# Kernel tuning notes

Measured on AMD Instinct MI355X. Metric: run time of the kernel, lower is better.

Reference implementation:

```python
import jax, jax.numpy as jnp
import numpy as np
from functools import partial

V, E, H, F = 32000, 256, 512, 256  # vocab, embed_dim, hidden_dim, num_filters
FS = (3, 4, 5)

def setup_inputs() -> dict:
    key = jax.random.key(0)
    ks = jax.random.split(key, 24)
    s = 0.02
    d = {}
    d["src"] = jax.random.randint(ks[0], (32, 512), 0, V)
    d["trg"] = jax.random.randint(ks[1], (32, 64), 0, V)
    # embeddings with padding_idx=0 zeroed
    d["enc_emb"] = (jax.random.normal(ks[2], (V, E)) * s).at[0].set(0.0)
    d["dec_emb"] = (jax.random.normal(ks[3], (V, E)) * s).at[0].set(0.0)
    # conv1d weights (out_channels=F, in_channels=E, kernel)
    d["conv_w3"] = jax.random.normal(ks[4], (F, E, 3)) * s
    d["conv_b3"] = jnp.zeros((F,))
    d["conv_w4"] = jax.random.normal(ks[5], (F, E, 4)) * s
    d["conv_b4"] = jnp.zeros((F,))
    d["conv_w5"] = jax.random.normal(ks[6], (F, E, 5)) * s
    d["conv_b5"] = jnp.zeros((F,))
    d["fc1_w"] = jax.random.normal(ks[7], (H, 3 * F)) * s
    d["fc1_b"] = jnp.zeros((H,))
    d["fc2_w"] = jax.random.normal(ks[8], (H, H)) * s
    d["fc2_b"] = jnp.zeros((H,))
    # 2-layer LSTM: layer1 input E+H, layer2 input H; gates order i,f,g,o
    d["w_ih1"] = jax.random.normal(ks[9], (4 * H, E + H)) * s
    d["w_hh1"] = jax.random.normal(ks[10], (4 * H, H)) * s
    d["b_ih1"] = jnp.zeros((4 * H,))
    d["b_hh1"] = jnp.zeros((4 * H,))
    d["w_ih2"] = jax.random.normal(ks[11], (4 * H, H)) * s
    d["w_hh2"] = jax.random.normal(ks[12], (4 * H, H)) * s
    d["b_ih2"] = jnp.zeros((4 * H,))
    d["b_hh2"] = jnp.zeros((4 * H,))
    d["out_w"] = jax.random.normal(ks[13], (V, H)) * s
    d["out_b"] = jnp.zeros((V,))
    return d

def _lstm_cell(x, h, c, w_ih, w_hh, b_ih, b_hh):
    gates = x @ w_ih.T + b_ih + h @ w_hh.T + b_hh  # (B, 4H)
    i, f, g, o = jnp.split(gates, 4, axis=-1)
    c_new = jax.nn.sigmoid(f) * c + jax.nn.sigmoid(i) * jnp.tanh(g)
    h_new = jax.nn.sigmoid(o) * jnp.tanh(c_new)
    return h_new, c_new

def _encoder(src, enc_emb, convs, fc1_w, fc1_b, fc2_w, fc2_b):
    x = enc_emb[src]                    # (B, S, E)
    x = jnp.transpose(x, (0, 2, 1))     # (B, E, S)
    pooled = []
    for w, b in convs:
        y = jax.lax.conv_general_dilated(
            x, w, window_strides=(1,), padding='VALID',
            dimension_numbers=('NCH', 'OIH', 'NCH'))  # (B, F, S-k+1)
        pooled.append(jnp.max(jax.nn.relu(y + b[None, :, None]), axis=2))
    cat = jnp.concatenate(pooled, axis=1)              # (B, 3F)
    h = jax.nn.relu(cat @ fc1_w.T + fc1_b)             # (B, H)
    return h @ fc2_w.T + fc2_b                         # (B, H)

def reference(src, trg, enc_emb, conv_w3, conv_b3, conv_w4, conv_b4,
              conv_w5, conv_b5, fc1_w, fc1_b, fc2_w, fc2_b, dec_emb,
              w_ih1, w_hh1, b_ih1, b_hh1, w_ih2, w_hh2, b_ih2, b_hh2,
              out_w, out_b):
    B, T = trg.shape
    enc_out = _encoder(src, enc_emb,
                       [(conv_w3, conv_b3), (conv_w4, conv_b4), (conv_w5, conv_b5)],
                       fc1_w, fc1_b, fc2_w, fc2_b)  # (B, H)

    def step(carry, tok):
        h1, c1, h2, c2 = carry
        x = jnp.concatenate([dec_emb[tok], enc_out], axis=1)  # (B, E+H)
        h1, c1 = _lstm_cell(x, h1, c1, w_ih1, w_hh1, b_ih1, b_hh1)
        h2, c2 = _lstm_cell(h1, h2, c2, w_ih2, w_hh2, b_ih2, b_hh2)
        logits = h2 @ out_w.T + out_b                          # (B, V)
        return (h1, c1, h2, c2), logits

    z = jnp.zeros((B, H), dtype=enc_out.dtype)
    tokens = trg[:, :-1].T  # teacher forcing (ratio=1.0): (T-1, B)
    _, logits = jax.lax.scan(step, (z, z, z, z), tokens)       # (T-1, B, V)
    logits = jnp.transpose(logits, (1, 0, 2))                  # (B, T-1, V)
    # outputs[:, 0] is left as zeros, matching the torch loop starting at t=1
    return jnp.concatenate([jnp.zeros((B, 1, logits.shape[-1]), logits.dtype), logits], axis=1)
```

## Files before the change

kernel.cpp:

```cpp
#include <hip/hip_runtime.h>
#include <math.h>
#include <stdint.h>

#define B_    32
#define E_    256
#define F_    256
#define H_    512
#define V_    32000
#define G4    2048

typedef unsigned short u16;
typedef unsigned long long u64;
typedef __attribute__((ext_vector_type(8))) short bf16x8;
typedef __attribute__((ext_vector_type(4))) float f32x4;

__device__ __forceinline__ float fsig(float x) {
  return __builtin_amdgcn_rcpf(1.f + __expf(-x));
}
__device__ __forceinline__ float ftanh(float x) {
  return 1.f - 2.f * __builtin_amdgcn_rcpf(1.f + __expf(2.f * x));
}

__device__ __forceinline__ u16 f2bf(float f) {
  uint32_t u = __float_as_uint(f);
  uint32_t r = (u + 0x7FFFu + ((u >> 16) & 1u)) >> 16;
  return (u16)r;
}
__device__ __forceinline__ uint32_t pack2(float a, float b) {
  return (uint32_t)f2bf(a) | ((uint32_t)f2bf(b) << 16);
}

#define GLOAD16(gp, lp) __builtin_amdgcn_global_load_lds( \
    (const __attribute__((address_space(1))) uint32_t*)(const void*)(gp), \
    (__attribute__((address_space(3))) uint32_t*)(void*)(lp), 16, 0, 0)

#define ALOAD(P) __hip_atomic_load((P), __ATOMIC_RELAXED, __HIP_MEMORY_SCOPE_AGENT)
#define ASTORE(P, V) __hip_atomic_store((P), (V), __ATOMIC_RELAXED, __HIP_MEMORY_SCOPE_AGENT)

__global__ void init_all(float* pooled, uint32_t* sent1, uint32_t* sent2,
                         uint32_t* cnt1, u16* h1d, u16* h2a,
                         const float* bi1, const float* bh1,
                         const float* bi2, const float* bh2,
                         float* bs1, float* bs2, float* out) {
  int i = blockIdx.x * blockDim.x + threadIdx.x, st = gridDim.x * blockDim.x;
  for (int k = i; k < 24576; k += st) pooled[k] = 0.f;
  for (int k = i; k < 131072; k += st) {
    uint32_t v = (k < 2048 && (k & 15) == 0) ? 1u : 0u;
    sent1[k] = v; sent2[k] = v;
  }
  for (int k = i; k < 256; k += st) cnt1[k] = 0u;
  uint4 z = {0u, 0u, 0u, 0u};
  for (int k = i; k < 2048; k += st) { ((uint4*)h1d)[k] = z; ((uint4*)h2a)[k] = z; }
  for (int k = i; k < G4; k += st) { bs1[k] = bi1[k] + bh1[k]; bs2[k] = bi2[k] + bh2[k]; }
  for (int k = i; k < B_ * V_; k += st) {
    int b = k / V_, v = k - b * V_;
    __builtin_nontemporal_store(0.f, &out[(size_t)b * 64 * V_ + v]);
  }
}

__global__ void cvt_all(const float* s0, u16* d0, const float* s1, u16* d1,
                        const float* s2, u16* d2, const float* s3, u16* d3,
                        const float* s4, u16* d4) {
  int i = blockIdx.x * blockDim.x + threadIdx.x, st = gridDim.x * blockDim.x;
  for (; i < 2637824; i += st) {
    int j = i; const float* s; u16* d;
    if (j < 2048000) { s = s0; d = d0; }
    else if ((j -= 2048000) < 196608) { s = s1; d = d1; }
    else if ((j -= 196608) < 131072) { s = s2; d = d2; }
    else if ((j -= 131072) < 131072) { s = s3; d = d3; }
    else { j -= 131072; s = s4; d = d4; }
    const float4* sp = (const float4*)s + 2 * (size_t)j;
    float4 a = sp[0], b = sp[1];
    uint4 u;
    u.x = pack2(a.x, a.y); u.y = pack2(a.z, a.w);
    u.z = pack2(b.x, b.y); u.w = pack2(b.z, b.w);
    *((uint4*)d + j) = u;
  }
}

__global__ void wtj_all(const float* w3, u16* t3, const float* w4, u16* t4,
                        const float* w5, u16* t5) {
  int i = blockIdx.x * blockDim.x + threadIdx.x, st = gridDim.x * blockDim.x;
  for (; i < 786432; i += st) {
    int j = i; const float* w; u16* wt; int kw;
    if (j < 196608) { w = w3; wt = t3; kw = 3; }
    else if ((j -= 196608) < 262144) { w = w4; wt = t4; kw = 4; }
    else { j -= 262144; w = w5; wt = t5; kw = 5; }
    int f = j / (kw * 256);
    int r = j - f * (kw * 256);
    int jj = r >> 8, e = r & 255;
    wt[j] = f2bf(w[(f * 256 + e) * kw + jj]);
  }
}

__global__ void gemm_small(const float* __restrict__ A, const float* __restrict__ W,
                           const float* __restrict__ bias, float* __restrict__ C,
                           int K, int N, int relu) {
  int nl = threadIdx.x & 7, b = threadIdx.x >> 3;
  int n = blockIdx.x * 8 + nl;
  const float* a = A + b * K;
  const float* w = W + (size_t)n * K;
  float acc = 0.f;
  for (int k = 0; k < K; k += 4) {
    float4 av = *reinterpret_cast<const float4*>(&a[k]);
    float4 wv = *reinterpret_cast<const float4*>(&w[k]);
    acc = fmaf(av.x, wv.x, acc); acc = fmaf(av.y, wv.y, acc);
    acc = fmaf(av.z, wv.z, acc); acc = fmaf(av.w, wv.w, acc);
  }
  acc += bias[n];
  if (relu) acc = fmaxf(acc, 0.f);
  C[b * N + n] = acc;
}

__global__ __launch_bounds__(256)
void conv_mfma(const u16* __restrict__ wt3, const u16* __restrict__ wt4,
               const u16* __restrict__ wt5,
               const float* __restrict__ cb3, const float* __restrict__ cb4,
               const float* __restrict__ cb5,
               float* __restrict__ pooled,
               const int* __restrict__ srcTok, const float* __restrict__ emb) {
  const int z = blockIdx.z;
  const u16* Bw = (z == 0) ? wt3 : (z == 1) ? wt4 : wt5;
  const float* bias = (z == 0) ? cb3 : (z == 1) ? cb4 : cb5;
  const int K = 768 + 256 * z, kw = 3 + z, poolOff = 256 * z;

  __shared__ char smem[32768];
  const int tid = threadIdx.x;
  const int wid = tid >> 6, lane = tid & 63;
  const int hi = lane >> 4, lo = lane & 15;
  const int wr = wid >> 1, wc = wid & 1;
  const int m0 = blockIdx.x * 128, n0 = blockIdx.y * 128;
  const int NT = K >> 5;
  const int srow = lane >> 2, sc = lane & 3;

  f32x4 acc[4][4];
#pragma unroll
  for (int i = 0; i < 4; ++i)
#pragma unroll
    for (int j = 0; j < 4; ++j) acc[i][j] = (f32x4){0.f, 0.f, 0.f, 0.f};

  for (int t = -1; t < NT; ++t) {
    int ts = t + 1;
    if (ts < NT) {
      char* base = smem + (ts & 1) * 16384;
      int k0 = ts << 5;
      {
        int j = k0 >> 8, e0 = k0 & 255;
        int row = tid >> 1;
        int m = m0 + row;
        int s = m & 511, b = m >> 9;
        int sj = s + j;
        int tok = (sj < 512) ? srcTok[b * 512 + sj] : -1;
#pragma unroll
        for (int q = 0; q < 2; ++q) {
          int cg = (tid & 1) * 2 + q;
          uint4 u;
          if (tok >= 0) {
            const float* ep = emb + (size_t)tok * 256 + e0 + cg * 8;
            float4 f0 = *(const float4*)(ep);
            float4 f1 = *(const float4*)(ep + 4);
            u.x = pack2(f0.x, f0.y); u.y = pack2(f0.z, f0.w);
            u.z = pack2(f1.x, f1.y); u.w = pack2(f1.z, f1.w);
          } else u = (uint4){0, 0, 0, 0};
          int c = cg ^ (row & 3);
          *(uint4*)(base + row * 64 + c * 16) = u;
        }
      }
#pragma unroll
      for (int q = 0; q < 2; ++q) {
        int row = (wid + q * 4) * 16 + srow;
        int gc = sc ^ (row & 3);
        const char* gp = (const char*)Bw + (((size_t)(n0 + row) * K + k0) << 1) + gc * 16;
        GLOAD16(gp, base + 8192 + (wid + q * 4) * 1024);
      }
    }
    if (t >= 0) {
      char* base = smem + (t & 1) * 16384;
      bf16x8 af[4], bfr[4];
#pragma unroll
      for (int mi = 0; mi < 4; ++mi) {
        int row = wr * 64 + mi * 16 + lo;
        af[mi] = *(const bf16x8*)(base + row * 64 + ((hi ^ (row & 3)) << 4));
      }
#pragma unroll
      for (int ni = 0; ni < 4; ++ni) {
        int row = wc * 64 + ni * 16 + lo;
        bfr[ni] = *(const bf16x8*)(base + 8192 + row * 64 + ((hi ^ (row & 3)) << 4));
      }
#pragma unroll
      for (int mi = 0; mi < 4; ++mi)
#pragma unroll
        for (int ni = 0; ni < 4; ++ni)
          acc[mi][ni] = __builtin_amdgcn_mfma_f32_16x16x32_bf16(af[mi], bfr[ni], acc[mi][ni], 0, 0, 0);
    }
    __syncthreads();
  }

  int b = m0 >> 9;
  int slim = 512 - kw;
#pragma unroll
  for (int ni = 0; ni < 4; ++ni) {
    int col = n0 + wc * 64 + ni * 16 + lo;
    float bv = bias[col];
    float mx = 0.f;
#pragma unroll
    for (int mi = 0; mi < 4; ++mi)
#pragma unroll
      for (int r = 0; r < 4; ++r) {
        int m = m0 + wr * 64 + mi * 16 + hi * 4 + r;
        int s = m & 511;
        float v = acc[mi][ni][r] + bv;
        if (s <= slim && v > mx) mx = v;
      }
    atomicMax((int*)&pooled[b * 768 + poolOff + col], __float_as_int(mx));
  }
}

__global__ __launch_bounds__(256, 1)
void lstm_fused(float* __restrict__ pre,
                const u16* __restrict__ whh1,
                const u16* __restrict__ wih2, const u16* __restrict__ whh2,
                const float* __restrict__ bs2,
                uint32_t* __restrict__ sent1, uint32_t* __restrict__ sent2,
                uint32_t* __restrict__ cnt1,
                u16* __restrict__ h1d, u16* __restrict__ h2a,
                const u16* __restrict__ outw_bf, const float* __restrict__ outb,
                float* __restrict__ out,
                const int* __restrict__ trg, const float* __restrict__ demb,
                const float* __restrict__ enco,
                const u16* __restrict__ wih1_bf, const float* __restrict__ bs1) {
  __shared__ char smem[74752];
  const int tid = threadIdx.x;
  const int wid = tid >> 6, lane = tid & 63, hi = lane >> 4, lo = lane & 15;
  const int hrow = tid >> 3, k8 = tid & 7;
  const int pb = hrow, pj0 = k8 * 2;

#define WAVE_DRAIN() asm volatile("s_waitcnt vmcnt(0)" ::: "memory")
#define POLL1(P) while (ALOAD(P) == 0u) __builtin_amdgcn_s_sleep(1);
#define POLL2(P, Q) for (;;) { uint32_t x_ = ALOAD(P), y_ = ALOAD(Q); \
                               if (x_ & y_) break; __builtin_amdgcn_s_sleep(1); }
#define POLL2S(P, Q) for (;;) { uint32_t x_ = ALOAD(P), y_ = ALOAD(Q); \
                                if (x_ & y_) break; __builtin_amdgcn_s_sleep(16); }

  if (blockIdx.x < 32) {
    const int bi = blockIdx.x;
    u16* hlds = (u16*)smem;
    float* glds = (float*)(smem + 33280);

    bf16x8 wreg[16];
    const u16* wp = whh1 + (((size_t)(wid * 512 + bi * 16 + lo)) << 9) + hi * 8;
#pragma unroll
    for (int ks = 0; ks < 16; ++ks) wreg[ks] = *(const bf16x8*)(wp + ks * 32);

    float creg0 = 0.f, creg1 = 0.f;

    for (int t = 0; t < 63; ++t) {
      if ((t & 3) == 0) {
        if (tid == 0)
          while (ALOAD(cnt1 + (t >> 2) * 16) < 16u) __builtin_amdgcn_s_sleep(8);
        __syncthreads();
      }
      const float* pr = pre + (((size_t)(t * 32 + pb)) << 11) + bi * 16 + pj0;
      float pi0 = pr[0], pf0 = pr[512], pg0 = pr[1024], po0 = pr[1536];
      float pi1 = pr[1], pf1 = pr[513], pg1 = pr[1025], po1 = pr[1537];

      const u64* hp = (const u64*)(h1d + ((size_t)t * 32 + hrow) * 512);
      f32x4 acc0 = (f32x4){0.f,0.f,0.f,0.f}, acc1 = (f32x4){0.f,0.f,0.f,0.f};

      POLL1(sent1 + (size_t)t * 2048 + lane * 16)
      {
        u64 v[8];
#pragma unroll
        for (int g = 0; g < 4; ++g) {
          int c = k8 + 8 * g;
          v[2*g]   = ALOAD(hp + 2 * c);
          v[2*g+1] = ALOAD(hp + 2 * c + 1);
        }
#pragma unroll
        for (int g = 0; g < 4; ++g) {
          int c = k8 + 8 * g;
          u64 w2[2] = { v[2*g], v[2*g+1] };
          *(uint4*)(hlds + hrow * 520 + c * 8) = *(const uint4*)w2;
        }
      }
      __syncthreads();
#pragma unroll
      for (int ks = 0; ks < 8; ++ks) {
        int cg = (ks * 4 + hi) * 8;
        bf16x8 a0 = *(const bf16x8*)(hlds + lo * 520 + cg);
        bf16x8 a1 = *(const bf16x8*)(hlds + (16 + lo) * 520 + cg);
        acc0 = __builtin_amdgcn_mfma_f32_16x16x32_bf16(a0, wreg[ks], acc0, 0, 0, 0);
        acc1 = __builtin_amdgcn_mfma_f32_16x16x32_bf16(a1, wreg[ks], acc1, 0, 0, 0);
      }
      POLL1(sent1 + (size_t)t * 2048 + (64 + lane) * 16)
      {
        u64 v[8];
#pragma unroll
        for (int g = 0; g < 4; ++g) {
          int c = 32 + k8 + 8 * g;
          v[2*g]   = ALOAD(hp + 2 * c);
          v[2*g+1] = ALOAD(hp + 2 * c + 1);
        }
#pragma unroll
        for (int g = 0; g < 4; ++g) {
          int c = 32 + k8 + 8 * g;
          u64 w2[2] = { v[2*g], v[2*g+1] };
          *(uint4*)(hlds + hrow * 520 + c * 8) = *(const uint4*)w2;
        }
      }
      __syncthreads();
#pragma unroll
      for (int ks = 8; ks < 16; ++ks) {
        int cg = (ks * 4 + hi) * 8;
        bf16x8 a0 = *(const bf16x8*)(hlds + lo * 520 + cg);
        bf16x8 a1 = *(const bf16x8*)(hlds + (16 + lo) * 520 + cg);
        acc0 = __builtin_amdgcn_mfma_f32_16x16x32_bf16(a0, wreg[ks], acc0, 0, 0, 0);
        acc1 = __builtin_amdgcn_mfma_f32_16x16x32_bf16(a1, wreg[ks], acc1, 0, 0, 0);
      }
#pragma unroll
      for (int r = 0; r < 4; ++r) {
        glds[wid * 544 + (hi * 4 + r) * 17 + lo] = acc0[r];
        glds[wid * 544 + (16 + hi * 4 + r) * 17 + lo] = acc1[r];
      }
      __syncthreads();

      float iv0 = glds[0*544 + pb*17 + pj0]   + pi0, fv0 = glds[1*544 + pb*17 + pj0]   + pf0;
      float gv0 = glds[2*544 + pb*17 + pj0]   + pg0, ov0 = glds[3*544 + pb*17 + pj0]   + po0;
      float iv1 = glds[0*544 + pb*17 + pj0+1] + pi1, fv1 = glds[1*544 + pb*17 + pj0+1] + pf1;
      float gv1 = glds[2*544 + pb*17 + pj0+1] + pg1, ov1 = glds[3*544 + pb*17 + pj0+1] + po1;
      float cn0 = fsig(fv0) * creg0 + fsig(iv0) * ftanh(gv0);
      float hn0 = fsig(ov0) * ftanh(cn0);
      float cn1 = fsig(fv1) * creg1 + fsig(iv1) * ftanh(gv1);
      float hn1 = fsig(ov1) * ftanh(cn1);
      creg0 = cn0; creg1 = cn1;
      ASTORE((uint32_t*)(h1d + ((size_t)(t + 1) * 32 + pb) * 512 + bi * 16 + pj0),
             pack2(hn0, hn1));
      WAVE_DRAIN();
      if (lane == 0)
        ASTORE(sent1 + (size_t)(t + 1) * 2048 + (bi * 4 + wid) * 16, 1u);
    }
  } else if (blockIdx.x < 64) {
    const int bi2 = blockIdx.x - 32;
    u16* alds = (u16*)smem;
    float* glds = (float*)(smem + 66048);

    bf16x8 wreg[32];
    {
      const u16* wa = wih2 + (((size_t)(wid * 512 + bi2 * 16 + lo)) << 9) + hi * 8;
      const u16* wb = whh2 + (((size_t)(wid * 512 + bi2 * 16 + lo)) << 9) + hi * 8;
#pragma unroll
      for (int ks = 0; ks < 16; ++ks) {
        wreg[ks]      = *(const bf16x8*)(wa + ks * 32);
        wreg[16 + ks] = *(const bf16x8*)(wb + ks * 32);
      }
    }
    float bsv0 = bs2[0 * 512 + bi2 * 16 + pj0], bsv0b = bs2[0 * 512 + bi2 * 16 + pj0 + 1];
    float bsv1 = bs2[1 * 512 + bi2 * 16 + pj0], bsv1b = bs2[1 * 512 + bi2 * 16 + pj0 + 1];
    float bsv2 = bs2[2 * 512 + bi2 * 16 + pj0], bsv2b = bs2[2 * 512 + bi2 * 16 + pj0 + 1];
    float bsv3 = bs2[3 * 512 + bi2 * 16 + pj0], bsv3b = bs2[3 * 512 + bi2 * 16 + pj0 + 1];

    float creg0 = 0.f, creg1 = 0.f;

    for (int t = 0; t < 63; ++t) {
      f32x4 acc0 = (f32x4){0.f,0.f,0.f,0.f}, acc1 = (f32x4){0.f,0.f,0.f,0.f};

      POLL2(sent1 + (size_t)(t + 1) * 2048 + lane * 16,
            sent1 + (size_t)(t + 1) * 2048 + (64 + lane) * 16)
      {
        const u64* hp1 = (const u64*)(h1d + ((size_t)(t + 1) * 32 + hrow) * 512);
        u64 v[16];
#pragma unroll
        for (int g = 0; g < 8; ++g) {
          int c = k8 + 8 * g;
          v[2*g]   = ALOAD(hp1 + 2 * c);
          v[2*g+1] = ALOAD(hp1 + 2 * c + 1);
        }
#pragma unroll
        for (int g = 0; g < 8; ++g) {
          int c = k8 + 8 * g;
          u64 w2[2] = { v[2*g], v[2*g+1] };
          *(uint4*)(alds + hrow * 1032 + c * 8) = *(const uint4*)w2;
        }
      }
      __syncthreads();
#pragma unroll
      for (int ks = 0; ks < 16; ++ks) {
        int cg = (ks * 4 + hi) * 8;
        bf16x8 a0 = *(const bf16x8*)(alds + lo * 1032 + cg);
        bf16x8 a1 = *(const bf16x8*)(alds + (16 + lo) * 1032 + cg);
        acc0 = __builtin_amdgcn_mfma_f32_16x16x32_bf16(a0, wreg[ks], acc0, 0, 0, 0);
        acc1 = __builtin_amdgcn_mfma_f32_16x16x32_bf16(a1, wreg[ks], acc1, 0, 0, 0);
      }
      POLL2(sent2 + (size_t)t * 2048 + lane * 16,
            sent2 + (size_t)t * 2048 + (64 + lane) * 16)
      {
        const u64* hp2 = (const u64*)(h2a + ((size_t)t * 32 + hrow) * 512);
        u64 v[16];
#pragma unroll
        for (int g = 0; g < 8; ++g) {
          int c = k8 + 8 * g;
          v[2*g]   = ALOAD(hp2 + 2 * c);
          v[2*g+1] = ALOAD(hp2 + 2 * c + 1);
        }
#pragma unroll
        for (int g = 0; g < 8; ++g) {
          int c = 64 + k8 + 8 * g;
          u64 w2[2] = { v[2*g], v[2*g+1] };
          *(uint4*)(alds + hrow * 1032 + c * 8) = *(const uint4*)w2;
        }
      }
      __syncthreads();
#pragma unroll
      for (int ks = 0; ks < 16; ++ks) {
        int cg = (64 + ks * 4 + hi) * 8;
        bf16x8 a0 = *(const bf16x8*)(alds + lo * 1032 + cg);
        bf16x8 a1 = *(const bf16x8*)(alds + (16 + lo) * 1032 + cg);
        acc0 = __builtin_amdgcn_mfma_f32_16x16x32_bf16(a0, wreg[16 + ks], acc0, 0, 0, 0);
        acc1 = __builtin_amdgcn_mfma_f32_16x16x32_bf16(a1, wreg[16 + ks], acc1, 0, 0, 0);
      }
#pragma unroll
      for (int r = 0; r < 4; ++r) {
        glds[wid * 544 + (hi * 4 + r) * 17 + lo] = acc0[r];
        glds[wid * 544 + (16 + hi * 4 + r) * 17 + lo] = acc1[r];
      }
      __syncthreads();

      float gi0 = glds[0*544 + pb*17 + pj0]   + bsv0,  gf0 = glds[1*544 + pb*17 + pj0]   + bsv1;
      float gg0 = glds[2*544 + pb*17 + pj0]   + bsv2,  go0 = glds[3*544 + pb*17 + pj0]   + bsv3;
      float gi1 = glds[0*544 + pb*17 + pj0+1] + bsv0b, gf1 = glds[1*544 + pb*17 + pj0+1] + bsv1b;
      float gg1 = glds[2*544 + pb*17 + pj0+1] + bsv2b, go1 = glds[3*544 + pb*17 + pj0+1] + bsv3b;
      float cn0 = fsig(gf0) * creg0 + fsig(gi0) * ftanh(gg0);
      float hn0 = fsig(go0) * ftanh(cn0);
      float cn1 = fsig(gf1) * creg1 + fsig(gi1) * ftanh(gg1);
      float hn1 = fsig(go1) * ftanh(cn1);
      creg0 = cn0; creg1 = cn1;
      ASTORE((uint32_t*)(h2a + ((size_t)(t + 1) * 32 + pb) * 512 + bi2 * 16 + pj0),
             pack2(hn0, hn1));
      WAVE_DRAIN();
      if (lane == 0)
        ASTORE(sent2 + (size_t)(t + 1) * 2048 + (bi2 * 4 + wid) * 16, 1u);
    }
  } else {
    const int bid2 = blockIdx.x - 64;
    const int wr = wid >> 1, wc = wid & 1;
    const int srow = lane >> 2, sc = lane & 3;

    for (int w = bid2; w < 256; w += 160) {
      int rt = w >> 4, ct = w & 15;
      const int m0 = rt * 128, n0 = ct * 128;
      f32x4 acc[4][4];
#pragma unroll
      for (int i = 0; i < 4; ++i)
#pragma unroll
        for (int j = 0; j < 4; ++j) acc[i][j] = (f32x4){0.f, 0.f, 0.f, 0.f};

      for (int t = -1; t < 24; ++t) {
        int ts = t + 1;
        if (ts < 24) {
          char* base = smem + (ts & 1) * 16384;
          int k0 = ts << 5;
          {
            int row = tid >> 1;
            int m = m0 + row;
            int tt = m >> 5, b = m & 31;
            int ok = (m < 2016);
            int tok = ok ? trg[b * 64 + tt] : 0;
#pragma unroll
            for (int q = 0; q < 2; ++q) {
              int cg = (tid & 1) * 2 + q;
              int k = k0 + cg * 8;
              uint4 u;
              if (ok) {
                const float* ep = (k < 256) ? (demb + (size_t)tok * 256 + k)
                                            : (enco + (size_t)b * 512 + (k - 256));
                float4 f0 = *(const float4*)(ep);
                float4 f1 = *(const float4*)(ep + 4);
                u.x = pack2(f0.x, f0.y); u.y = pack2(f0.z, f0.w);
                u.z = pack2(f1.x, f1.y); u.w = pack2(f1.z, f1.w);
              } else u = (uint4){0, 0, 0, 0};
              int c = cg ^ (row & 3);
              *(uint4*)(base + row * 64 + c * 16) = u;
            }
          }
#pragma unroll
          for (int q = 0; q < 2; ++q) {
            int row = (wid + q * 4) * 16 + srow;
            int gc = sc ^ (row & 3);
            const char* gp = (const char*)wih1_bf + (((size_t)(n0 + row) * 768 + k0) << 1) + gc * 16;
            GLOAD16(gp, base + 8192 + (wid + q * 4) * 1024);
          }
        }
        if (t >= 0) {
          char* base = smem + (t & 1) * 16384;
          bf16x8 af[4], bfr[4];
#pragma unroll
          for (int mi = 0; mi < 4; ++mi) {
            int row = wr * 64 + mi * 16 + lo;
            af[mi] = *(const bf16x8*)(base + row * 64 + ((hi ^ (row & 3)) << 4));
          }
#pragma unroll
          for (int ni = 0; ni < 4; ++ni) {
            int row = wc * 64 + ni * 16 + lo;
            bfr[ni] = *(const bf16x8*)(base + 8192 + row * 64 + ((hi ^ (row & 3)) << 4));
          }
#pragma unroll
          for (int mi = 0; mi < 4; ++mi)
#pragma unroll
            for (int ni = 0; ni < 4; ++ni)
              acc[mi][ni] = __builtin_amdgcn_mfma_f32_16x16x32_bf16(af[mi], bfr[ni], acc[mi][ni], 0, 0, 0);
        }
        __syncthreads();
      }
#pragma unroll
      for (int mi = 0; mi < 4; ++mi)
#pragma unroll
        for (int r = 0; r < 4; ++r) {
          int m = m0 + wr * 64 + mi * 16 + hi * 4 + r;
          if (m >= 2016) continue;
#pragma unroll
          for (int ni = 0; ni < 4; ++ni) {
            int col = n0 + wc * 64 + ni * 16 + lo;
            ASTORE((uint32_t*)(pre + (size_t)m * 2048 + col),
                   __float_as_uint(acc[mi][ni][r] + bs1[col]));
          }
        }
      WAVE_DRAIN();
      __syncthreads();
      if (tid == 0)
        __hip_atomic_fetch_add(cnt1 + rt * 16, 1u, __ATOMIC_RELAXED, __HIP_MEMORY_SCOPE_AGENT);
      __syncthreads();
    }

    const u16* A = h2a + 16384;

    for (int w = bid2; w < 16 * 250; w += 160) {
      int rt = w / 250, ct = w - rt * 250;
      int tf = rt * 4 + 4; if (tf > 63) tf = 63;
      if (wid == 0)
        POLL2S(sent2 + (size_t)tf * 2048 + lane * 16,
               sent2 + (size_t)tf * 2048 + (64 + lane) * 16)
      __syncthreads();

      const int m0 = rt * 128, n0 = ct * 128;
      f32x4 acc[4][4];
#pragma unroll
      for (int i = 0; i < 4; ++i)
#pragma unroll
        for (int j = 0; j < 4; ++j) acc[i][j] = (f32x4){0.f, 0.f, 0.f, 0.f};

      for (int t = -1; t < 16; ++t) {
        int ts = t + 1;
        if (ts < 16) {
          char* base = smem + (ts & 1) * 16384;
          int k0 = ts << 5;
#pragma unroll
          for (int q = 0; q < 2; ++q) {
            int row = (wid + q * 4) * 16 + srow;
            int gc = sc ^ (row & 3);
            const char* gp = (const char*)A + (((size_t)(m0 + row) * 512 + k0) << 1) + gc * 16;
            GLOAD16(gp, base + (wid + q * 4) * 1024);
          }
#pragma unroll
          for (int q = 0; q < 2; ++q) {
            int row = (wid + q * 4) * 16 + srow;
            int gc = sc ^ (row & 3);
            const char* gp = (const char*)outw_bf + (((size_t)(n0 + row) * 512 + k0) << 1) + gc * 16;
            GLOAD16(gp, base + 8192 + (wid + q * 4) * 1024);
          }
        }
        if (t >= 0) {
          char* base = smem + (t & 1) * 16384;
          bf16x8 af[4], bfr[4];
#pragma unroll
          for (int mi = 0; mi < 4; ++mi) {
            int row = wr * 64 + mi * 16 + lo;
            af[mi] = *(const bf16x8*)(base + row * 64 + ((hi ^ (row & 3)) << 4));
          }
#pragma unroll
          for (int ni = 0; ni < 4; ++ni) {
            int row = wc * 64 + ni * 16 + lo;
            bfr[ni] = *(const bf16x8*)(base + 8192 + row * 64 + ((hi ^ (row & 3)) << 4));
          }
#pragma unroll
          for (int mi = 0; mi < 4; ++mi)
#pragma unroll
            for (int ni = 0; ni < 4; ++ni)
              acc[mi][ni] = __builtin_amdgcn_mfma_f32_16x16x32_bf16(af[mi], bfr[ni], acc[mi][ni], 0, 0, 0);
        }
        __syncthreads();
      }

#pragma unroll
      for (int mi = 0; mi < 4; ++mi)
#pragma unroll
        for (int r = 0; r < 4; ++r) {
          int m = m0 + wr * 64 + mi * 16 + hi * 4 + r;
          if (m >= 2016) continue;
          int t2 = m >> 5, b = m & 31;
          size_t rowbase = ((size_t)b * 64 + t2 + 1) * (size_t)V_;
#pragma unroll
          for (int ni = 0; ni < 4; ++ni) {
            int col = n0 + wc * 64 + ni * 16 + lo;
            __builtin_nontemporal_store(acc[mi][ni][r] + outb[col], &out[rowbase + col]);
          }
        }
    }
  }
#undef POLL1
#undef POLL2
#undef POLL2S
#undef WAVE_DRAIN
}

extern "C" void kernel_launch(void* const* d_in, const int* in_sizes, int n_in,
                              void* d_out, int out_size, void* d_ws, size_t ws_size,
                              hipStream_t stream) {
  const int*   src  = (const int*)  d_in[0];
  const int*   trg  = (const int*)  d_in[1];
  const float* eemb = (const float*)d_in[2];
  const float* demb = (const float*)d_in[3];
  const float* cw3  = (const float*)d_in[4];
  const float* cb3  = (const float*)d_in[5];
  const float* cw4  = (const float*)d_in[6];
  const float* cb4  = (const float*)d_in[7];
  const float* cw5  = (const float*)d_in[8];
  const float* cb5  = (const float*)d_in[9];
  const float* fc1w = (const float*)d_in[10];
  const float* fc1b = (const float*)d_in[11];
  const float* fc2w = (const float*)d_in[12];
  const float* fc2b = (const float*)d_in[13];
  const float* wih1 = (const float*)d_in[14];
  const float* whh1 = (const float*)d_in[15];
  const float* bih1 = (const float*)d_in[16];
  const float* bhh1 = (const float*)d_in[17];
  const float* wih2 = (const float*)d_in[18];
  const float* whh2 = (const float*)d_in[19];
  const float* bih2 = (const float*)d_in[20];
  const float* bhh2 = (const float*)d_in[21];
  const float* outw = (const float*)d_in[22];
  const float* outb = (const float*)d_in[23];
  float* out = (float*)d_out;

  uint32_t* sent1 = (uint32_t*)d_ws;
  uint32_t* sent2 = sent1 + 131072;
  uint32_t* cnt1  = sent2 + 131072;
  u16* h1d      = (u16*)(cnt1 + 256);
  u16* h2a      = h1d + 1048576;
  float* pooled = (float*)(h2a + 1048576);
  float* ench   = pooled + 24576;
  float* enco   = ench + 16384;
  float* bs1    = enco + 16384;
  float* bs2    = bs1 + 2048;
  float* pre    = bs2 + 2048;
  u16* outw_bf  = (u16*)(pre + 4128768);
  u16* wih1_bf  = outw_bf + 16384000;
  u16* wih2_bf  = wih1_bf + 1572864;
  u16* whh1_bf  = wih2_bf + 1048576;
  u16* whh2_bf  = whh1_bf + 1048576;
  u16* wtj3     = whh2_bf + 1048576;
  u16* wtj4     = wtj3 + 196608;
  u16* wtj5     = wtj4 + 262144;

  init_all<<<512, 256, 0, stream>>>(pooled, sent1, sent2, cnt1, h1d, h2a,
                                    bih1, bhh1, bih2, bhh2, bs1, bs2, out);
  cvt_all<<<2048, 256, 0, stream>>>(outw, outw_bf, wih1, wih1_bf, wih2, wih2_bf,
                                    whh1, whh1_bf, whh2, whh2_bf);
  wtj_all<<<512, 256, 0, stream>>>(cw3, wtj3, cw4, wtj4, cw5, wtj5);

  conv_mfma<<<dim3(128, 2, 3), 256, 0, stream>>>(wtj3, wtj4, wtj5, cb3, cb4, cb5,
                                                 pooled, src, eemb);
  gemm_small<<<64, 256, 0, stream>>>(pooled, fc1w, fc1b, ench, 768, 512, 1);
  gemm_small<<<64, 256, 0, stream>>>(ench, fc2w, fc2b, enco, 512, 512, 0);

  lstm_fused<<<224, 256, 0, stream>>>(pre, whh1_bf, wih2_bf, whh2_bf, bs2,
                                      sent1, sent2, cnt1, h1d, h2a,
                                      outw_bf, outb, out,
                                      trg, demb, enco, wih1_bf, bs1);
}
```

Baseline: 467.3 us.

## Merge prep kernels and make output-GEMM blocks own column tiles

Result: slower. 576.7 us (+23.4%).

```diff
diff --git a/kernel.cpp b/kernel.cpp
--- a/kernel.cpp
+++ b/kernel.cpp
@@ -37,33 +37,19 @@
 #define ALOAD(P) __hip_atomic_load((P), __ATOMIC_RELAXED, __HIP_MEMORY_SCOPE_AGENT)
 #define ASTORE(P, V) __hip_atomic_store((P), (V), __ATOMIC_RELAXED, __HIP_MEMORY_SCOPE_AGENT)
 
-__global__ void init_all(float* pooled, uint32_t* sent1, uint32_t* sent2,
+__global__ void prep_all(float* pooled, uint32_t* sent1, uint32_t* sent2,
                          uint32_t* cnt1, u16* h1d, u16* h2a,
                          const float* bi1, const float* bh1,
                          const float* bi2, const float* bh2,
-                         float* bs1, float* bs2, float* out) {
+                         float* bs1, float* bs2, float* out,
+                         const float* s0, u16* d0, const float* s1, u16* d1,
+                         const float* s2, u16* d2, const float* s3, u16* d3,
+                         const float* s4, u16* d4,
+                         const float* w3, u16* t3, const float* w4, u16* t4,
+                         const float* w5, u16* t5) {
   int i = blockIdx.x * blockDim.x + threadIdx.x, st = gridDim.x * blockDim.x;
-  for (int k = i; k < 24576; k += st) pooled[k] = 0.f;
-  for (int k = i; k < 131072; k += st) {
-    uint32_t v = (k < 2048 && (k & 15) == 0) ? 1u : 0u;
-    sent1[k] = v; sent2[k] = v;
-  }
-  for (int k = i; k < 256; k += st) cnt1[k] = 0u;
-  uint4 z = {0u, 0u, 0u, 0u};
-  for (int k = i; k < 2048; k += st) { ((uint4*)h1d)[k] = z; ((uint4*)h2a)[k] = z; }
-  for (int k = i; k < G4; k += st) { bs1[k] = bi1[k] + bh1[k]; bs2[k] = bi2[k] + bh2[k]; }
-  for (int k = i; k < B_ * V_; k += st) {
-    int b = k / V_, v = k - b * V_;
-    __builtin_nontemporal_store(0.f, &out[(size_t)b * 64 * V_ + v]);
-  }
-}
-
-__global__ void cvt_all(const float* s0, u16* d0, const float* s1, u16* d1,
-                        const float* s2, u16* d2, const float* s3, u16* d3,
-                        const float* s4, u16* d4) {
-  int i = blockIdx.x * blockDim.x + threadIdx.x, st = gridDim.x * blockDim.x;
-  for (; i < 2637824; i += st) {
-    int j = i; const float* s; u16* d;
+  for (int k = i; k < 2637824; k += st) {
+    int j = k; const float* s; u16* d;
     if (j < 2048000) { s = s0; d = d0; }
     else if ((j -= 2048000) < 196608) { s = s1; d = d1; }
     else if ((j -= 196608) < 131072) { s = s2; d = d2; }
@@ -76,13 +62,8 @@
     u.z = pack2(b.x, b.y); u.w = pack2(b.z, b.w);
     *((uint4*)d + j) = u;
   }
-}
-
-__global__ void wtj_all(const float* w3, u16* t3, const float* w4, u16* t4,
-                        const float* w5, u16* t5) {
-  int i = blockIdx.x * blockDim.x + threadIdx.x, st = gridDim.x * blockDim.x;
-  for (; i < 786432; i += st) {
-    int j = i; const float* w; u16* wt; int kw;
+  for (int k = i; k < 786432; k += st) {
+    int j = k; const float* w; u16* wt; int kw;
     if (j < 196608) { w = w3; wt = t3; kw = 3; }
     else if ((j -= 196608) < 262144) { w = w4; wt = t4; kw = 4; }
     else { j -= 262144; w = w5; wt = t5; kw = 5; }
@@ -90,6 +71,19 @@
     int r = j - f * (kw * 256);
     int jj = r >> 8, e = r & 255;
     wt[j] = f2bf(w[(f * 256 + e) * kw + jj]);
+  }
+  for (int k = i; k < 24576; k += st) pooled[k] = 0.f;
+  for (int k = i; k < 131072; k += st) {
+    uint32_t v = (k < 2048 && (k & 15) == 0) ? 1u : 0u;
+    sent1[k] = v; sent2[k] = v;
+  }
+  for (int k = i; k < 256; k += st) cnt1[k] = 0u;
+  uint4 z = {0u, 0u, 0u, 0u};
+  for (int k = i; k < 2048; k += st) { ((uint4*)h1d)[k] = z; ((uint4*)h2a)[k] = z; }
+  for (int k = i; k < G4; k += st) { bs1[k] = bi1[k] + bh1[k]; bs2[k] = bi2[k] + bh2[k]; }
+  for (int k = i; k < B_ * V_; k += st) {
+    int b = k / V_, v = k - b * V_;
+    __builtin_nontemporal_store(0.f, &out[(size_t)b * 64 * V_ + v]);
   }
 }
 
@@ -533,77 +527,78 @@
 
     const u16* A = h2a + 16384;
 
-    for (int w = bid2; w < 16 * 250; w += 160) {
-      int rt = w / 250, ct = w - rt * 250;
-      int tf = rt * 4 + 4; if (tf > 63) tf = 63;
-      if (wid == 0)
-        POLL2S(sent2 + (size_t)tf * 2048 + lane * 16,
-               sent2 + (size_t)tf * 2048 + (64 + lane) * 16)
-      __syncthreads();
-
-      const int m0 = rt * 128, n0 = ct * 128;
-      f32x4 acc[4][4];
-#pragma unroll
-      for (int i = 0; i < 4; ++i)
-#pragma unroll
-        for (int j = 0; j < 4; ++j) acc[i][j] = (f32x4){0.f, 0.f, 0.f, 0.f};
-
-      for (int t = -1; t < 16; ++t) {
-        int ts = t + 1;
-        if (ts < 16) {
-          char* base = smem + (ts & 1) * 16384;
-          int k0 = ts << 5;
-#pragma unroll
-          for (int q = 0; q < 2; ++q) {
-            int row = (wid + q * 4) * 16 + srow;
-            int gc = sc ^ (row & 3);
-            const char* gp = (const char*)A + (((size_t)(m0 + row) * 512 + k0) << 1) + gc * 16;
-            GLOAD16(gp, base + (wid + q * 4) * 1024);
-          }
-#pragma unroll
-          for (int q = 0; q < 2; ++q) {
-            int row = (wid + q * 4) * 16 + srow;
-            int gc = sc ^ (row & 3);
-            const char* gp = (const char*)outw_bf + (((size_t)(n0 + row) * 512 + k0) << 1) + gc * 16;
-            GLOAD16(gp, base + 8192 + (wid + q * 4) * 1024);
-          }
-        }
-        if (t >= 0) {
-          char* base = smem + (t & 1) * 16384;
-          bf16x8 af[4], bfr[4];
-#pragma unroll
-          for (int mi = 0; mi < 4; ++mi) {
-            int row = wr * 64 + mi * 16 + lo;
-            af[mi] = *(const bf16x8*)(base + row * 64 + ((hi ^ (row & 3)) << 4));
-          }
-#pragma unroll
-          for (int ni = 0; ni < 4; ++ni) {
-            int row = wc * 64 + ni * 16 + lo;
-            bfr[ni] = *(const bf16x8*)(base + 8192 + row * 64 + ((hi ^ (row & 3)) << 4));
-          }
-#pragma unroll
-          for (int mi = 0; mi < 4; ++mi)
-#pragma unroll
-            for (int ni = 0; ni < 4; ++ni)
-              acc[mi][ni] = __builtin_amdgcn_mfma_f32_16x16x32_bf16(af[mi], bfr[ni], acc[mi][ni], 0, 0, 0);
-        }
+    for (int ct = bid2; ct < 250; ct += 160) {
+      for (int rt = 0; rt < 16; ++rt) {
+        int tf = rt * 4 + 4; if (tf > 63) tf = 63;
+        if (wid == 0)
+          POLL2S(sent2 + (size_t)tf * 2048 + lane * 16,
+                 sent2 + (size_t)tf * 2048 + (64 + lane) * 16)
         __syncthreads();
-      }
-
-#pragma unroll
-      for (int mi = 0; mi < 4; ++mi)
-#pragma unroll
-        for (int r = 0; r < 4; ++r) {
-          int m = m0 + wr * 64 + mi * 16 + hi * 4 + r;
-          if (m >= 2016) continue;
-          int t2 = m >> 5, b = m & 31;
-          size_t rowbase = ((size_t)b * 64 + t2 + 1) * (size_t)V_;
-#pragma unroll
-          for (int ni = 0; ni < 4; ++ni) {
-            int col = n0 + wc * 64 + ni * 16 + lo;
-            __builtin_nontemporal_store(acc[mi][ni][r] + outb[col], &out[rowbase + col]);
-          }
-        }
+
+        const int m0 = rt * 128, n0 = ct * 128;
+        f32x4 acc[4][4];
+#pragma unroll
+        for (int i = 0; i < 4; ++i)
+#pragma unroll
+          for (int j = 0; j < 4; ++j) acc[i][j] = (f32x4){0.f, 0.f, 0.f, 0.f};
+
+        for (int t = -1; t < 16; ++t) {
+          int ts = t + 1;
+          if (ts < 16) {
+            char* base = smem + (ts & 1) * 16384;
+            int k0 = ts << 5;
+#pragma unroll
+            for (int q = 0; q < 2; ++q) {
+              int row = (wid + q * 4) * 16 + srow;
+              int gc = sc ^ (row & 3);
+              const char* gp = (const char*)A + (((size_t)(m0 + row) * 512 + k0) << 1) + gc * 16;
+              GLOAD16(gp, base + (wid + q * 4) * 1024);
+            }
+#pragma unroll
+            for (int q = 0; q < 2; ++q) {
+              int row = (wid + q * 4) * 16 + srow;
+              int gc = sc ^ (row & 3);
+              const char* gp = (const char*)outw_bf + (((size_t)(n0 + row) * 512 + k0) << 1) + gc * 16;
+              GLOAD16(gp, base + 8192 + (wid + q * 4) * 1024);
+            }
+          }
+          if (t >= 0) {
+            char* base = smem + (t & 1) * 16384;
+            bf16x8 af[4], bfr[4];
+#pragma unroll
+            for (int mi = 0; mi < 4; ++mi) {
+              int row = wr * 64 + mi * 16 + lo;
+              af[mi] = *(const bf16x8*)(base + row * 64 + ((hi ^ (row & 3)) << 4));
+            }
+#pragma unroll
+            for (int ni = 0; ni < 4; ++ni) {
+              int row = wc * 64 + ni * 16 + lo;
+              bfr[ni] = *(const bf16x8*)(base + 8192 + row * 64 + ((hi ^ (row & 3)) << 4));
+            }
+#pragma unroll
+            for (int mi = 0; mi < 4; ++mi)
+#pragma unroll
+              for (int ni = 0; ni < 4; ++ni)
+                acc[mi][ni] = __builtin_amdgcn_mfma_f32_16x16x32_bf16(af[mi], bfr[ni], acc[mi][ni], 0, 0, 0);
+          }
+          __syncthreads();
+        }
+
+#pragma unroll
+        for (int mi = 0; mi < 4; ++mi)
+#pragma unroll
+          for (int r = 0; r < 4; ++r) {
+            int m = m0 + wr * 64 + mi * 16 + hi * 4 + r;
+            if (m >= 2016) continue;
+            int t2 = m >> 5, b = m & 31;
+            size_t rowbase = ((size_t)b * 64 + t2 + 1) * (size_t)V_;
+#pragma unroll
+            for (int ni = 0; ni < 4; ++ni) {
+              int col = n0 + wc * 64 + ni * 16 + lo;
+              __builtin_nontemporal_store(acc[mi][ni][r] + outb[col], &out[rowbase + col]);
+            }
+          }
+      }
     }
   }
 #undef POLL1
@@ -661,11 +656,11 @@
   u16* wtj4     = wtj3 + 196608;
   u16* wtj5     = wtj4 + 262144;
 
-  init_all<<<512, 256, 0, stream>>>(pooled, sent1, sent2, cnt1, h1d, h2a,
-                                    bih1, bhh1, bih2, bhh2, bs1, bs2, out);
-  cvt_all<<<2048, 256, 0, stream>>>(outw, outw_bf, wih1, wih1_bf, wih2, wih2_bf,
-                                    whh1, whh1_bf, whh2, whh2_bf);
-  wtj_all<<<512, 256, 0, stream>>>(cw3, wtj3, cw4, wtj4, cw5, wtj5);
+  prep_all<<<1024, 256, 0, stream>>>(pooled, sent1, sent2, cnt1, h1d, h2a,
+                                     bih1, bhh1, bih2, bhh2, bs1, bs2, out,
+                                     outw, outw_bf, wih1, wih1_bf, wih2, wih2_bf,
+                                     whh1, whh1_bf, whh2, whh2_bf,
+                                     cw3, wtj3, cw4, wtj4, cw5, wtj5);
 
   conv_mfma<<<dim3(128, 2, 3), 256, 0, stream>>>(wtj3, wtj4, wtj5, cb3, cb4, cb5,
                                                  pooled, src, eemb);
```
